# Kernel tuning notes

Measured on AMD Instinct MI355X. Metric: run time of the kernel, lower is better.

The kernel has to match this reference:

```python
import jax, jax.numpy as jnp
import numpy as np

BN_EPS = 1e-5

def tanhshrink(x):
    return x - jnp.tanh(x)

def setup_inputs() -> dict:
    key = jax.random.key(0)
    ks = jax.random.split(key, 10)
    B, C, H, W = 32, 128, 32, 32
    RIN, RH, OC = 256, 512, 128
    s = lambda k, shape, fan: jax.random.normal(k, shape, dtype=jnp.float32) * (1.0 / np.sqrt(fan))
    return {
        "x": jax.random.normal(ks[0], (B, C, H, W), dtype=jnp.float32),
        "gamma": jnp.ones((C,), jnp.float32),
        "beta": jnp.zeros((C,), jnp.float32),
        "w_in": s(ks[1], (RIN, C), C),
        "b_in": jnp.zeros((RIN,), jnp.float32),
        "w_ih": s(ks[2], (RH, RIN), RIN),
        "b_ih": jnp.zeros((RH,), jnp.float32),
        "w_hh": s(ks[3], (RH, RH), RH),
        "b_hh": jnp.zeros((RH,), jnp.float32),
        "w_out": s(ks[4], (OC, RH), RH),
        "b_out": jnp.zeros((OC,), jnp.float32),
    }

def reference(x, gamma, beta, w_in, b_in, w_ih, b_ih, w_hh, b_hh, w_out, b_out):
    B, C, H, W = x.shape
    RH = w_hh.shape[0]
    # BatchNorm2d (training mode: batch statistics, biased variance)
    mean = jnp.mean(x, axis=(0, 2, 3), keepdims=True)
    var = jnp.var(x, axis=(0, 2, 3), keepdims=True)
    xn = (x - mean) * jax.lax.rsqrt(var + BN_EPS)
    xn = xn * gamma[None, :, None, None] + beta[None, :, None, None]
    # (B, L, C) sequence of flattened spatial locations
    seq = jnp.transpose(xn, (0, 2, 3, 1)).reshape(B, H * W, C)
    # Per-timestep Linear + Tanhshrink: has no recurrence, batch it over L
    inp = tanhshrink(jnp.einsum('blc,ic->bli', seq, w_in) + b_in)  # (B, L, RIN)
    # Precompute input contribution to RNNCell for all steps
    xgate = jnp.einsum('bli,hi->blh', inp, w_ih) + b_ih + b_hh  # (B, L, RH)
    xgate_t = jnp.transpose(xgate, (1, 0, 2))  # (L, B, RH)

    def step(h, xg):
        h_new = jnp.tanh(xg + h @ w_hh.T)
        return h_new, h_new

    h0 = jnp.zeros((B, RH), x.dtype)
    _, hs = jax.lax.scan(step, h0, xgate_t)  # (L, B, RH)
    outputs = jnp.transpose(hs, (1, 0, 2))  # (B, L, RH)
    out_seq = jnp.einsum('blh,oh->blo', outputs, w_out) + b_out  # (B, L, OC)
    out = jnp.transpose(out_seq.reshape(B, H, W, -1), (0, 3, 1, 2))
    return out
```

## Files before the change

kernel.cpp:

```cpp
#include <hip/hip_runtime.h>
#include <hip/hip_fp16.h>

typedef _Float16 f16;
typedef _Float16 f16x2 __attribute__((ext_vector_type(2)));
typedef _Float16 f16x8 __attribute__((ext_vector_type(8)));
typedef float    f32x4 __attribute__((ext_vector_type(4)));
typedef unsigned int u32;
typedef unsigned long long u64;

#define BN_EPS 1e-5f

static constexpr int BB  = 32;
static constexpr int CC  = 128;
static constexpr int HWN = 1024;
static constexpr int RIN = 256;
static constexpr int RH  = 512;
static constexpr int OCN = 128;

__global__ void bn_stats_kernel(const float* __restrict__ x,
                                const float* __restrict__ gamma,
                                const float* __restrict__ beta,
                                float* __restrict__ scale,
                                float* __restrict__ shift) {
    int c = blockIdx.x;
    int tid = threadIdx.x;
    float s = 0.f, s2 = 0.f;
    const float* xc = x + (size_t)c * HWN;
    for (int idx = tid; idx < BB * HWN; idx += 256) {
        int b = idx >> 10, hw = idx & 1023;
        float v = xc[(size_t)b * (CC * HWN) + hw];
        s += v; s2 += v * v;
    }
    for (int off = 32; off > 0; off >>= 1) {
        s  += __shfl_down(s, off, 64);
        s2 += __shfl_down(s2, off, 64);
    }
    __shared__ float ls[4], ls2[4];
    int wv = tid >> 6, ln = tid & 63;
    if (ln == 0) { ls[wv] = s; ls2[wv] = s2; }
    __syncthreads();
    if (tid == 0) {
        float ts  = ls[0] + ls[1] + ls[2] + ls[3];
        float ts2 = ls2[0] + ls2[1] + ls2[2] + ls2[3];
        const float inv_n = 1.0f / (BB * HWN);
        float mean = ts * inv_n;
        float var  = ts2 * inv_n - mean * mean;
        float rstd = rsqrtf(var + BN_EPS);
        float sc = gamma[c] * rstd;
        scale[c] = sc;
        shift[c] = beta[c] - mean * sc;
    }
}

__global__ void prep_x_kernel(const float* __restrict__ x,
                              const float* __restrict__ scale,
                              const float* __restrict__ shift,
                              f16* __restrict__ A1) {
    __shared__ float tile[32][33];
    int tx = threadIdx.x, ty = threadIdx.y;
    int hb = blockIdx.x, cb = blockIdx.y, b = blockIdx.z;
    #pragma unroll
    for (int k = 0; k < 4; k++) {
        int c  = cb * 32 + ty + 8 * k;
        int hw = hb * 32 + tx;
        tile[ty + 8 * k][tx] = x[(size_t)b * (CC * HWN) + (size_t)c * HWN + hw];
    }
    __syncthreads();
    #pragma unroll
    for (int k = 0; k < 4; k++) {
        int hw = hb * 32 + ty + 8 * k;
        int c  = cb * 32 + tx;
        float v = tile[tx][ty + 8 * k];
        A1[(size_t)(b * HWN + hw) * CC + c] = (f16)(v * scale[c] + shift[c]);
    }
}

__global__ void prep_w_kernel(const float* __restrict__ w_in,
                              const float* __restrict__ w_ih,
                              const float* __restrict__ w_out,
                              const float* __restrict__ w_hh,
                              const float* __restrict__ b_ih,
                              const float* __restrict__ b_hh,
                              f16* __restrict__ w_in_h,
                              f16* __restrict__ w_ih_h,
                              f16* __restrict__ w_out_h,
                              u32* __restrict__ wr,
                              float* __restrict__ bihh,
                              u64* __restrict__ comm) {
    int idx = blockIdx.x * 256 + threadIdx.x;
    if (idx < 32768) { w_in_h[idx] = (f16)w_in[idx]; return; }
    idx -= 32768;
    if (idx < 131072) { w_ih_h[idx] = (f16)w_ih[idx]; return; }
    idx -= 131072;
    if (idx < 65536) { w_out_h[idx] = (f16)w_out[idx]; return; }
    idx -= 65536;
    if (idx < 131072) {
        int s = idx >> 15, rem = idx & 32767;
        int t = rem >> 6, k = rem & 63;
        int r = k >> 4, n = k & 15;
        int jg = t & 31, sl = t >> 5;
        int j  = s * 128 + 4 * jg + r;
        int i2 = sl * 16 + n;
        f16 lo = (f16)w_hh[(size_t)j * 512 + 2 * i2];
        f16 hi = (f16)w_hh[(size_t)j * 512 + 2 * i2 + 1];
        wr[idx] = (u32)__builtin_bit_cast(unsigned short, lo) |
                  ((u32)__builtin_bit_cast(unsigned short, hi) << 16);
        return;
    }
    idx -= 131072;
    if (idx < 512) { bihh[idx] = b_ih[idx] + b_hh[idx]; return; }
    idx -= 512;
    if (idx < 16384) comm[idx] = 0ULL;
}

template <int MODE>
__global__ void gemm_kernel(const f16* __restrict__ A,
                            const f16* __restrict__ W,
                            const float* __restrict__ bias,
                            void* __restrict__ outp,
                            int N, int K) {
    int wave = threadIdx.x >> 6;
    int lane = threadIdx.x & 63;
    int q = lane >> 4, r = lane & 15;
    int bm = blockIdx.x * 256 + wave * 64;
    int bn = blockIdx.y * 64;

    f32x4 acc[4][4];
    #pragma unroll
    for (int i = 0; i < 4; i++)
        #pragma unroll
        for (int j = 0; j < 4; j++)
            acc[i][j] = (f32x4){0.f, 0.f, 0.f, 0.f};

    const f16* Ap = A + (size_t)(bm + r) * K + 8 * q;
    const f16* Wp = W + (size_t)(bn + r) * K + 8 * q;

    for (int k = 0; k < K; k += 32) {
        f16x8 av[4], bv[4];
        #pragma unroll
        for (int i = 0; i < 4; i++)
            av[i] = *(const f16x8*)(Ap + (size_t)(16 * i) * K + k);
        #pragma unroll
        for (int i = 0; i < 4; i++)
            bv[i] = *(const f16x8*)(Wp + (size_t)(16 * i) * K + k);
        #pragma unroll
        for (int mi = 0; mi < 4; mi++)
            #pragma unroll
            for (int ni = 0; ni < 4; ni++)
                acc[mi][ni] = __builtin_amdgcn_mfma_f32_16x16x32_f16(
                    av[mi], bv[ni], acc[mi][ni], 0, 0, 0);
    }

    #pragma unroll
    for (int mi = 0; mi < 4; mi++) {
        #pragma unroll
        for (int ni = 0; ni < 4; ni++) {
            int col = bn + 16 * ni + r;
            float bval = bias[col];
            #pragma unroll
            for (int i = 0; i < 4; i++) {
                int row = bm + 16 * mi + 4 * q + i;
                float val = acc[mi][ni][i] + bval;
                if (MODE == 0) {
                    val = val - tanhf(val);
                    ((f16*)outp)[(size_t)row * N + col] = (f16)val;
                } else if (MODE == 1) {
                    ((f16*)outp)[(size_t)row * N + col] = (f16)val;
                } else {
                    int b = row >> 10, hw = row & 1023;
                    ((float*)outp)[(size_t)b * (OCN * HWN) + (size_t)col * HWN + hw] = val;
                }
            }
        }
    }
}

__device__ __forceinline__ float dot2acc(u32 w, f16x2 h, float c) {
#if __has_builtin(__builtin_amdgcn_fdot2)
    return __builtin_amdgcn_fdot2(__builtin_bit_cast(f16x2, w), h, c, false);
#else
    f16x2 a = __builtin_bit_cast(f16x2, w);
    return c + (float)a[0] * (float)h[0] + (float)a[1] * (float)h[1];
#endif
}

__global__ __launch_bounds__(512) void rnn_kernel(const u32* __restrict__ WR,
                                                  f16* __restrict__ xh,
                                                  u64* __restrict__ comm) {
    const int wg = blockIdx.x;
    const int b  = wg & 31;
    const int s  = wg >> 5;
    const int t  = threadIdx.x;
    const int jg = t & 31;
    const int sl = t >> 5;

    __shared__ __align__(16) f16 hbuf[512];
    __shared__ float part[16][128];

    u32 w[64];
    {
        const uint4* wp = (const uint4*)(WR + ((size_t)(s * 512 + t) << 6));
        #pragma unroll
        for (int i = 0; i < 16; i++) {
            uint4 v = wp[i];
            w[4*i+0] = v.x; w[4*i+1] = v.y; w[4*i+2] = v.z; w[4*i+3] = v.w;
        }
    }
    if (t < 256) ((u32*)hbuf)[t] = 0u;
    __syncthreads();

    f16* xb = xh + (size_t)b * (HWN * RH) + s * 128;
    float xnext = 0.f;
    if (t < 128) xnext = (float)xb[t];

    u64* cb = comm + (size_t)b * 256;

    for (int step = 0; step < HWN; step++) {
        float xcur = xnext;
        if (t < 128 && step + 1 < HWN)
            xnext = (float)xb[(size_t)(step + 1) * RH + t];

        const uint4* hq = (const uint4*)hbuf;
        uint4 q0 = hq[sl*4+0], q1 = hq[sl*4+1], q2 = hq[sl*4+2], q3 = hq[sl*4+3];
        u32 hv[16] = {q0.x,q0.y,q0.z,q0.w, q1.x,q1.y,q1.z,q1.w,
                      q2.x,q2.y,q2.z,q2.w, q3.x,q3.y,q3.z,q3.w};
        float a0 = 0.f, a1 = 0.f, a2 = 0.f, a3 = 0.f;
        #pragma unroll
        for (int n = 0; n < 16; n++) {
            f16x2 hh = __builtin_bit_cast(f16x2, hv[n]);
            a0 = dot2acc(w[n],      hh, a0);
            a1 = dot2acc(w[16 + n], hh, a1);
            a2 = dot2acc(w[32 + n], hh, a2);
            a3 = dot2acc(w[48 + n], hh, a3);
        }
        *(f32x4*)&part[sl][4 * jg] = (f32x4){a0, a1, a2, a3};
        __syncthreads();

        const u32 tag = (u32)(step + 1);
        const size_t pbase = (size_t)(tag & 1) * 8192;

        if (t < 128) {
            float y = xcur;
            #pragma unroll
            for (int k = 0; k < 16; k++) y += part[k][t];
            float h = tanhf(y);
            f16 hf = (f16)h;
            u32 hu = (u32)__builtin_bit_cast(unsigned short, hf);
            u32 other = (u32)__shfl_down((int)hu, 1, 64);
            if ((t & 1) == 0) {
                u64 v = ((u64)tag << 32) | (u64)(hu | (other << 16));
                __hip_atomic_store(&cb[pbase + s * 64 + (t >> 1)], v,
                                   __ATOMIC_RELAXED, __HIP_MEMORY_SCOPE_AGENT);
            }
            hbuf[s * 128 + t] = hf;
            xb[(size_t)step * RH + t] = hf;
        }
        if (t < 192) {
            int pi = t >> 6;
            int widx = t & 63;
            int p = pi + (pi >= s ? 1 : 0);
            u64 v;
            int guard = 0;
            do {
                v = __hip_atomic_load(&cb[pbase + p * 64 + widx],
                                      __ATOMIC_RELAXED, __HIP_MEMORY_SCOPE_AGENT);
            } while ((u32)(v >> 32) != tag && ++guard < (1 << 17));
            ((u32*)hbuf)[p * 64 + widx] = (u32)v;
        }
        __syncthreads();
    }
}

extern "C" void kernel_launch(void* const* d_in, const int* in_sizes, int n_in,
                              void* d_out, int out_size, void* d_ws, size_t ws_size,
                              hipStream_t stream) {
    const float* x     = (const float*)d_in[0];
    const float* gamma = (const float*)d_in[1];
    const float* beta  = (const float*)d_in[2];
    const float* w_in  = (const float*)d_in[3];
    const float* b_in  = (const float*)d_in[4];
    const float* w_ih  = (const float*)d_in[5];
    const float* b_ih  = (const float*)d_in[6];
    const float* w_hh  = (const float*)d_in[7];
    const float* b_hh  = (const float*)d_in[8];
    const float* w_out = (const float*)d_in[9];
    const float* b_out = (const float*)d_in[10];

    char* ws = (char*)d_ws;
    float* scale   = (float*)(ws + 0);
    float* shift   = (float*)(ws + 512);
    float* bihh    = (float*)(ws + 1024);
    f16*   w_in_h  = (f16*)(ws + 4096);
    f16*   w_ih_h  = (f16*)(ws + 69632);
    f16*   w_out_h = (f16*)(ws + 331776);
    u32*   wr      = (u32*)(ws + 462848);
    u64*   comm    = (u64*)(ws + 987136);
    f16*   xh      = (f16*)(ws + 1179648);
    f16*   A1      = (f16*)(ws + 34734080);
    f16*   inp     = (f16*)(ws + 43122688);

    bn_stats_kernel<<<128, 256, 0, stream>>>(x, gamma, beta, scale, shift);
    prep_w_kernel<<<1474, 256, 0, stream>>>(w_in, w_ih, w_out, w_hh, b_ih, b_hh,
                                            w_in_h, w_ih_h, w_out_h, wr, bihh, comm);
    prep_x_kernel<<<dim3(32, 4, 32), dim3(32, 8), 0, stream>>>(x, scale, shift, A1);
    gemm_kernel<0><<<dim3(128, 4), 256, 0, stream>>>(A1, w_in_h, b_in, (void*)inp, RIN, CC);
    gemm_kernel<1><<<dim3(128, 8), 256, 0, stream>>>(inp, w_ih_h, bihh, (void*)xh, RH, RIN);
    rnn_kernel<<<128, 512, 0, stream>>>(wr, xh, comm);
    gemm_kernel<2><<<dim3(128, 2), 256, 0, stream>>>(xh, w_out_h, b_out, d_out, OCN, RH);
}
```

Before: 1.618 ms.

## Restructure RNN step with shuffle reduction, double-buffered h, and dual-scope flag polling

Changes the recurrent weight layout so that each group of four threads owns one output row, and reduces partial dot products with cross-lane shuffles instead of an LDS partial array plus a barrier. The hidden state in shared memory is double-buffered, which removes one __syncthreads per step. Inter-workgroup exchange now polls a workgroup-scope 'fast' mailbox through compare-exchange and falls back to an agent-scope mailbox, aiming to cut cross-CU latency per step. This relies on memory-scope behaviour that may not be well defined across workgroups, and it doubles the comm buffer.

```diff
diff --git a/kernel.cpp b/kernel.cpp
--- a/kernel.cpp
+++ b/kernel.cpp
@@ -97,10 +97,8 @@
     if (idx < 131072) {
         int s = idx >> 15, rem = idx & 32767;
         int t = rem >> 6, k = rem & 63;
-        int r = k >> 4, n = k & 15;
-        int jg = t & 31, sl = t >> 5;
-        int j  = s * 128 + 4 * jg + r;
-        int i2 = sl * 16 + n;
+        int j  = s * 128 + (t >> 2);
+        int i2 = (t & 3) * 64 + k;
         f16 lo = (f16)w_hh[(size_t)j * 512 + 2 * i2];
         f16 hi = (f16)w_hh[(size_t)j * 512 + 2 * i2 + 1];
         wr[idx] = (u32)__builtin_bit_cast(unsigned short, lo) |
@@ -110,7 +108,7 @@
     idx -= 131072;
     if (idx < 512) { bihh[idx] = b_ih[idx] + b_hh[idx]; return; }
     idx -= 512;
-    if (idx < 16384) comm[idx] = 0ULL;
+    if (idx < 32768) comm[idx] = 0ULL;
 }
 
 template <int MODE>
@@ -184,88 +182,107 @@
 #endif
 }
 
-__global__ __launch_bounds__(512) void rnn_kernel(const u32* __restrict__ WR,
-                                                  f16* __restrict__ xh,
-                                                  u64* __restrict__ comm) {
+#define QSTEP(hv, Wq, acc)                                          \
+    acc = dot2acc(Wq.x, __builtin_bit_cast(f16x2, hv.x), acc);      \
+    acc = dot2acc(Wq.y, __builtin_bit_cast(f16x2, hv.y), acc);      \
+    acc = dot2acc(Wq.z, __builtin_bit_cast(f16x2, hv.z), acc);      \
+    acc = dot2acc(Wq.w, __builtin_bit_cast(f16x2, hv.w), acc);
+
+__global__ __launch_bounds__(512, 2) void rnn_kernel(const u32* WR,
+                                                     f16* __restrict__ xh,
+                                                     u64* slow, u64* fast) {
     const int wg = blockIdx.x;
     const int b  = wg & 31;
     const int s  = wg >> 5;
     const int t  = threadIdx.x;
-    const int jg = t & 31;
-    const int sl = t >> 5;
-
-    __shared__ __align__(16) f16 hbuf[512];
-    __shared__ float part[16][128];
-
-    u32 w[64];
-    {
-        const uint4* wp = (const uint4*)(WR + ((size_t)(s * 512 + t) << 6));
-        #pragma unroll
-        for (int i = 0; i < 16; i++) {
-            uint4 v = wp[i];
-            w[4*i+0] = v.x; w[4*i+1] = v.y; w[4*i+2] = v.z; w[4*i+3] = v.w;
-        }
-    }
-    if (t < 256) ((u32*)hbuf)[t] = 0u;
+    const int row = t >> 2;
+    const int kq  = t & 3;
+
+    __shared__ __align__(16) u32 hbuf[2][256];
+
+    unsigned long long wpa =
+        (unsigned long long)(WR + ((size_t)(s * 512 + t) << 6));
+    asm volatile("" : "+v"(wpa));
+    const uint4* wp = (const uint4*)wpa;
+    uint4 W0 = wp[0],  W1 = wp[1],  W2 = wp[2],  W3 = wp[3];
+    uint4 W4 = wp[4],  W5 = wp[5],  W6 = wp[6],  W7 = wp[7];
+    uint4 W8 = wp[8],  W9 = wp[9],  W10 = wp[10], W11 = wp[11];
+    uint4 W12 = wp[12], W13 = wp[13], W14 = wp[14], W15 = wp[15];
+
+    if (t < 256) hbuf[0][t] = 0u;
     __syncthreads();
 
     f16* xb = xh + (size_t)b * (HWN * RH) + s * 128;
     float xnext = 0.f;
-    if (t < 128) xnext = (float)xb[t];
-
-    u64* cb = comm + (size_t)b * 256;
+    if ((t & 3) == 3) xnext = (float)xb[row];
+
+    u64* cbS = slow + (size_t)b * 256;
+    u64* cbF = fast + (size_t)b * 256;
 
     for (int step = 0; step < HWN; step++) {
-        float xcur = xnext;
-        if (t < 128 && step + 1 < HWN)
-            xnext = (float)xb[(size_t)(step + 1) * RH + t];
-
-        const uint4* hq = (const uint4*)hbuf;
-        uint4 q0 = hq[sl*4+0], q1 = hq[sl*4+1], q2 = hq[sl*4+2], q3 = hq[sl*4+3];
-        u32 hv[16] = {q0.x,q0.y,q0.z,q0.w, q1.x,q1.y,q1.z,q1.w,
-                      q2.x,q2.y,q2.z,q2.w, q3.x,q3.y,q3.z,q3.w};
-        float a0 = 0.f, a1 = 0.f, a2 = 0.f, a3 = 0.f;
-        #pragma unroll
-        for (int n = 0; n < 16; n++) {
-            f16x2 hh = __builtin_bit_cast(f16x2, hv[n]);
-            a0 = dot2acc(w[n],      hh, a0);
-            a1 = dot2acc(w[16 + n], hh, a1);
-            a2 = dot2acc(w[32 + n], hh, a2);
-            a3 = dot2acc(w[48 + n], hh, a3);
-        }
-        *(f32x4*)&part[sl][4 * jg] = (f32x4){a0, a1, a2, a3};
-        __syncthreads();
-
         const u32 tag = (u32)(step + 1);
         const size_t pbase = (size_t)(tag & 1) * 8192;
-
-        if (t < 128) {
-            float y = xcur;
-            #pragma unroll
-            for (int k = 0; k < 16; k++) y += part[k][t];
-            float h = tanhf(y);
-            f16 hf = (f16)h;
-            u32 hu = (u32)__builtin_bit_cast(unsigned short, hf);
-            u32 other = (u32)__shfl_down((int)hu, 1, 64);
-            if ((t & 1) == 0) {
-                u64 v = ((u64)tag << 32) | (u64)(hu | (other << 16));
-                __hip_atomic_store(&cb[pbase + s * 64 + (t >> 1)], v,
-                                   __ATOMIC_RELAXED, __HIP_MEMORY_SCOPE_AGENT);
-            }
-            hbuf[s * 128 + t] = hf;
-            xb[(size_t)step * RH + t] = hf;
+        const u32* hcur = hbuf[step & 1];
+        u32* hnext = hbuf[tag & 1];
+
+        const uint4* hqb = ((const uint4*)hcur) + kq * 16;
+        float a0 = 0.f, a1 = 0.f, a2 = 0.f, a3 = 0.f;
+        {
+            uint4 h0 = hqb[0],  h1 = hqb[1],  h2 = hqb[2],  h3 = hqb[3];
+            QSTEP(h0, W0, a0) QSTEP(h1, W1, a1) QSTEP(h2, W2, a2) QSTEP(h3, W3, a3)
+            uint4 h4 = hqb[4],  h5 = hqb[5],  h6 = hqb[6],  h7 = hqb[7];
+            QSTEP(h4, W4, a0) QSTEP(h5, W5, a1) QSTEP(h6, W6, a2) QSTEP(h7, W7, a3)
+            uint4 h8 = hqb[8],  h9 = hqb[9],  h10 = hqb[10], h11 = hqb[11];
+            QSTEP(h8, W8, a0) QSTEP(h9, W9, a1) QSTEP(h10, W10, a2) QSTEP(h11, W11, a3)
+            uint4 h12 = hqb[12], h13 = hqb[13], h14 = hqb[14], h15 = hqb[15];
+            QSTEP(h12, W12, a0) QSTEP(h13, W13, a1) QSTEP(h14, W14, a2) QSTEP(h15, W15, a3)
+        }
+        float y = (a0 + a1) + (a2 + a3);
+        y += __shfl_xor(y, 1, 64);
+        y += __shfl_xor(y, 2, 64);
+
+        f16 hf = (f16)0.f;
+        float xcur = xnext;
+        if ((t & 3) == 3) {
+            hf = (f16)tanhf(y + xcur);
+            if (step + 1 < HWN) xnext = (float)xb[(size_t)(step + 1) * RH + row];
+        }
+        u32 hu = (u32)__builtin_bit_cast(unsigned short, hf);
+        u32 hlo = (u32)__shfl_up((int)hu, 4, 64);
+
+        if ((t & 7) == 7) {
+            int w = t >> 3;
+            u32 word = hlo | (hu << 16);
+            hnext[s * 64 + w] = word;
+            ((u32*)(xb + (size_t)step * RH))[w] = word;
+            u64 v = ((u64)tag << 32) | (u64)word;
+            __hip_atomic_store(&cbF[pbase + s * 64 + w], v,
+                               __ATOMIC_RELAXED, __HIP_MEMORY_SCOPE_WORKGROUP);
+            __hip_atomic_store(&cbS[pbase + s * 64 + w], v,
+                               __ATOMIC_RELAXED, __HIP_MEMORY_SCOPE_AGENT);
         }
         if (t < 192) {
             int pi = t >> 6;
             int widx = t & 63;
             int p = pi + (pi >= s ? 1 : 0);
-            u64 v;
+            u64* aF = &cbF[pbase + p * 64 + widx];
+            u64* aS = &cbS[pbase + p * 64 + widx];
+            u64 exp = 0;
+            u32 pay;
             int guard = 0;
-            do {
-                v = __hip_atomic_load(&cb[pbase + p * 64 + widx],
-                                      __ATOMIC_RELAXED, __HIP_MEMORY_SCOPE_AGENT);
-            } while ((u32)(v >> 32) != tag && ++guard < (1 << 17));
-            ((u32*)hbuf)[p * 64 + widx] = (u32)v;
+            for (;;) {
+                u64 cur = exp;
+                __hip_atomic_compare_exchange_strong(
+                    aF, &cur, cur, __ATOMIC_RELAXED, __ATOMIC_RELAXED,
+                    __HIP_MEMORY_SCOPE_WORKGROUP);
+                if ((u32)(cur >> 32) == tag) { pay = (u32)cur; break; }
+                exp = cur;
+                u64 vs = __hip_atomic_load(aS, __ATOMIC_RELAXED,
+                                           __HIP_MEMORY_SCOPE_AGENT);
+                if ((u32)(vs >> 32) == tag) { pay = (u32)vs; break; }
+                if (++guard > (1 << 17)) { pay = (u32)vs; break; }
+            }
+            hnext[p * 64 + widx] = pay;
         }
         __syncthreads();
     }
@@ -294,17 +311,18 @@
     f16*   w_ih_h  = (f16*)(ws + 69632);
     f16*   w_out_h = (f16*)(ws + 331776);
     u32*   wr      = (u32*)(ws + 462848);
-    u64*   comm    = (u64*)(ws + 987136);
-    f16*   xh      = (f16*)(ws + 1179648);
-    f16*   A1      = (f16*)(ws + 34734080);
-    f16*   inp     = (f16*)(ws + 43122688);
+    u64*   cslow   = (u64*)(ws + 987136);
+    u64*   cfast   = (u64*)(ws + 1118208);
+    f16*   xh      = (f16*)(ws + 1310720);
+    f16*   A1      = (f16*)(ws + 34865152);
+    f16*   inp     = (f16*)(ws + 43253760);
 
     bn_stats_kernel<<<128, 256, 0, stream>>>(x, gamma, beta, scale, shift);
-    prep_w_kernel<<<1474, 256, 0, stream>>>(w_in, w_ih, w_out, w_hh, b_ih, b_hh,
-                                            w_in_h, w_ih_h, w_out_h, wr, bihh, comm);
+    prep_w_kernel<<<1538, 256, 0, stream>>>(w_in, w_ih, w_out, w_hh, b_ih, b_hh,
+                                            w_in_h, w_ih_h, w_out_h, wr, bihh, cslow);
     prep_x_kernel<<<dim3(32, 4, 32), dim3(32, 8), 0, stream>>>(x, scale, shift, A1);
     gemm_kernel<0><<<dim3(128, 4), 256, 0, stream>>>(A1, w_in_h, b_in, (void*)inp, RIN, CC);
     gemm_kernel<1><<<dim3(128, 8), 256, 0, stream>>>(inp, w_ih_h, bihh, (void*)xh, RH, RIN);
-    rnn_kernel<<<128, 512, 0, stream>>>(wr, xh, comm);
+    rnn_kernel<<<128, 512, 0, stream>>>(wr, xh, cslow, cfast);
     gemm_kernel<2><<<dim3(128, 2), 256, 0, stream>>>(xh, w_out_h, b_out, d_out, OCN, RH);
 }
```

Measured after the change: 2.444 ms. 1.51x slower.
